# Optimization experiments

Hardware: AMD Instinct MI355X
Metric: run time of the kernel (lower is better)

The kernel has to match this reference:

```python
import jax, jax.numpy as jnp
import numpy as np

ALPHA = 0.2   # leaky relu negative slope
EPS = 1e-5    # layernorm eps
NEG = -1e12   # mask value from original code


def gat_layer(x, adj, W, a):
    # x: [N, F_in], adj: [N, N] bool, W: [F_in, F_out], a: [2*F_out, 1]
    F_out = W.shape[1]
    Wh = x @ W                                  # [N, F_out]
    # a^T [Wh_i ; Wh_j] decomposes into f1_i + f2_j (same math as the
    # O(N^2 * 2F) concat in the torch code, without materializing it)
    f1 = Wh @ a[:F_out]                         # [N, 1]
    f2 = Wh @ a[F_out:]                         # [N, 1]
    e = jax.nn.leaky_relu(f1 + f2.T, negative_slope=ALPHA)  # [N, N]
    att = jnp.where(adj, e, NEG)
    att = jax.nn.softmax(att, axis=1)           # dropout p=0.0 -> no-op
    return att @ Wh                             # [N, F_out]


def layernorm(x, g, b):
    mu = jnp.mean(x, axis=-1, keepdims=True)
    var = jnp.var(x, axis=-1, keepdims=True)
    return (x - mu) * jax.lax.rsqrt(var + EPS) * g + b


def setup_inputs() -> dict:
    N, F = 8192, 128
    key = jax.random.key(0)
    ks = jax.random.split(key, 12)
    inp = {
        "input_hs": jax.random.normal(ks[0], (2, N, F), jnp.float32),
        "adjs": jax.random.uniform(ks[1], (2, N, N)) < 0.3,   # bool adjacency
        "MPNN_emb": jax.random.normal(ks[2], (N, F), jnp.float32),
        "query": jax.random.normal(ks[3], (1, F), jnp.float32),
        # learned params (xavier-ish scale)
        "W0": jax.random.normal(ks[4], (F, F), jnp.float32) * (1.414 / np.sqrt(F)),
        "a0": jax.random.normal(ks[5], (2 * F, 1), jnp.float32) * 0.1,
        "W1": jax.random.normal(ks[6], (F, F), jnp.float32) * (1.414 / np.sqrt(F)),
        "a1": jax.random.normal(ks[7], (2 * F, 1), jnp.float32) * 0.1,
        "ln_gamma": jnp.ones((F,), jnp.float32),
        "ln_beta": jnp.zeros((F,), jnp.float32),
        "res": jax.random.normal(ks[8], (1, 1), jnp.float32) * 0.5,
    }
    return inp


def reference(input_hs, adjs, MPNN_emb, query, W0, a0, W1, a1, ln_gamma, ln_beta, res):
    h0 = gat_layer(input_hs[0], adjs[0], W0, a0)   # [N, F]
    h1 = gat_layer(input_hs[1], adjs[1], W1, a1)   # [N, F]
    q = layernorm(query, ln_gamma, ln_beta)        # [1, F]
    w1 = q @ h0.T                                  # [1, N]
    w2 = q @ h1.T
    w3 = q @ MPNN_emb.T
    scores = jax.nn.softmax(jnp.concatenate([w1, w2, w3], axis=0), axis=0)  # [3, N]
    # diag_embed(s) @ H is just per-row scaling s[:, None] * H
    mix = (scores[0][:, None] * h0
           + scores[1][:, None] * h1
           + scores[2][:, None] * MPNN_emb)
    return res * mix + input_hs[0]
```

## Files before the change

### kernel.cpp

```cpp
#include <hip/hip_runtime.h>
#include <hip/hip_bf16.h>
#include <cstdint>


#define N 8192
#define F 128
#define JS 8

typedef __attribute__((ext_vector_type(8))) short short8;
typedef __attribute__((ext_vector_type(8))) unsigned short ushort8;
typedef __attribute__((ext_vector_type(4))) float floatx4;

__device__ inline unsigned int f2bf(float x) {
  unsigned int u = __float_as_uint(x);
  u += 0x7FFFu + ((u >> 16) & 1u);
  return u >> 16;
}


__global__ __launch_bounds__(128) void k1_wh(
    const float* __restrict__ X2, const float* __restrict__ W0,
    const float* __restrict__ W1, const float* __restrict__ a0,
    const float* __restrict__ a1, unsigned short* __restrict__ Whbt,
    float* __restrict__ f1g, float* __restrict__ f2g) {
  const int l  = blockIdx.y;
  const int i0 = blockIdx.x * 16;
  const int c  = threadIdx.x;
  const float* __restrict__ X = X2 + (size_t)l * N * F + (size_t)i0 * F;
  const float* __restrict__ W = l ? W1 : W0;

  __shared__ __align__(16) float sX[16 * F];
  __shared__ float red[2][2][16];
  {
    const float4* src = (const float4*)X;
    float4* dst = (float4*)sX;
#pragma unroll
    for (int qq = 0; qq < 4; ++qq) dst[qq * 128 + c] = src[qq * 128 + c];
  }
  __syncthreads();

  float acc[16];
#pragma unroll
  for (int r = 0; r < 16; ++r) acc[r] = 0.f;

  for (int f4 = 0; f4 < 32; ++f4) {
    float w0 = W[(f4 * 4 + 0) * F + c];
    float w1 = W[(f4 * 4 + 1) * F + c];
    float w2 = W[(f4 * 4 + 2) * F + c];
    float w3 = W[(f4 * 4 + 3) * F + c];
#pragma unroll
    for (int r = 0; r < 16; ++r) {
      float4 xv = *(const float4*)(&sX[r * F + f4 * 4]);
      acc[r] = fmaf(xv.x, w0, acc[r]);
      acc[r] = fmaf(xv.y, w1, acc[r]);
      acc[r] = fmaf(xv.z, w2, acc[r]);
      acc[r] = fmaf(xv.w, w3, acc[r]);
    }
  }

  {
    unsigned short* wdst = Whbt + (size_t)l * F * N + (size_t)c * N + i0;
    ushort8 u0, u1;
#pragma unroll
    for (int r = 0; r < 8; ++r) {
      u0[r] = (unsigned short)f2bf(acc[r]);
      u1[r] = (unsigned short)f2bf(acc[8 + r]);
    }
    *(ushort8*)wdst = u0;
    *(ushort8*)(wdst + 8) = u1;
  }

  const float* __restrict__ a = l ? a1 : a0;
  const float a1c = a[c], a2c = a[F + c];
  const int w = c >> 6, lane = c & 63;
#pragma unroll
  for (int r = 0; r < 16; ++r) {
    float s1 = acc[r] * a1c;
    float s2 = acc[r] * a2c;
#pragma unroll
    for (int off = 32; off; off >>= 1) {
      s1 += __shfl_down(s1, off);
      s2 += __shfl_down(s2, off);
    }
    if (lane == 0) {
      red[w][0][r] = s1;
      red[w][1][r] = s2;
    }
  }
  __syncthreads();
  if (c < 16)
    f1g[l * N + i0 + c] = red[0][0][c] + red[1][0][c];
  else if (c < 32)
    f2g[l * N + i0 + c - 16] = red[0][1][c - 16] + red[1][1][c - 16];
}

__global__ __launch_bounds__(128) void k3_qln(
    const float* __restrict__ query, const float* __restrict__ gamma,
    const float* __restrict__ beta, float* __restrict__ qln) {
  const int t = threadIdx.x;
  float v = query[t];
  float s = v, sq = v * v;
#pragma unroll
  for (int off = 32; off; off >>= 1) {
    s += __shfl_down(s, off);
    sq += __shfl_down(sq, off);
  }
  __shared__ float sb[4];
  if ((t & 63) == 0) {
    sb[t >> 6] = s;
    sb[2 + (t >> 6)] = sq;
  }
  __syncthreads();
  float S = sb[0] + sb[1], SQ = sb[2] + sb[3];
  float mu = S * (1.f / 128.f);
  float var = SQ * (1.f / 128.f) - mu * mu;
  qln[t] = (v - mu) * rsqrtf(var + 1e-5f) * gamma[t] + beta[t];
}

__device__ inline short8 make_pfrag(float f1v, const float4& fa,
                                    const float4& fb, const int4& a0,
                                    const int4& a1, float& Lacc) {
  float p0, p1, p2, p3, p4, p5, p6, p7, sc;
  sc = f1v + fa.x; sc = fmaxf(sc, 0.2f * sc); p0 = a0.x ? __expf(sc) : 0.f;
  sc = f1v + fa.y; sc = fmaxf(sc, 0.2f * sc); p1 = a0.y ? __expf(sc) : 0.f;
  sc = f1v + fa.z; sc = fmaxf(sc, 0.2f * sc); p2 = a0.z ? __expf(sc) : 0.f;
  sc = f1v + fa.w; sc = fmaxf(sc, 0.2f * sc); p3 = a0.w ? __expf(sc) : 0.f;
  sc = f1v + fb.x; sc = fmaxf(sc, 0.2f * sc); p4 = a1.x ? __expf(sc) : 0.f;
  sc = f1v + fb.y; sc = fmaxf(sc, 0.2f * sc); p5 = a1.y ? __expf(sc) : 0.f;
  sc = f1v + fb.z; sc = fmaxf(sc, 0.2f * sc); p6 = a1.z ? __expf(sc) : 0.f;
  sc = f1v + fb.w; sc = fmaxf(sc, 0.2f * sc); p7 = a1.w ? __expf(sc) : 0.f;
  Lacc += ((p0 + p1) + (p2 + p3)) + ((p4 + p5) + (p6 + p7));
  union { unsigned int u[4]; short8 s8; } r;
  r.u[0] = f2bf(p0) | (f2bf(p1) << 16);
  r.u[1] = f2bf(p2) | (f2bf(p3) << 16);
  r.u[2] = f2bf(p4) | (f2bf(p5) << 16);
  r.u[3] = f2bf(p6) | (f2bf(p7) << 16);
  return r.s8;
}

__global__ __launch_bounds__(256) void k2_attn(
    const unsigned short* __restrict__ Whbt, const float* __restrict__ f1g,
    const float* __restrict__ f2g, const int* __restrict__ adj,
    float* __restrict__ hpart, float* __restrict__ Lpart) {
  const int l  = blockIdx.y;
  const int s  = blockIdx.z;
  const int i0 = blockIdx.x * 128;
  const int t  = threadIdx.x;
  const int wave = t >> 6, lane = t & 63;
  const int lpos = lane & 15, halfk = lane >> 4;

  const unsigned short* __restrict__ WhbL = Whbt + (size_t)l * F * N;
  const int* __restrict__ adjL = adj + (size_t)l * N * N;
  const float* __restrict__ f2L = f2g + l * N;

  const int rowA = i0 + wave * 32 + lpos;
  const float f1a = f1g[l * N + rowA];
  const float f1b = f1g[l * N + rowA + 16];
  const int* __restrict__ adjA = adjL + (size_t)rowA * N + halfk * 8;
  const int* __restrict__ adjB = adjA + (size_t)16 * N;
  const unsigned short* __restrict__ bbase = WhbL + (size_t)lpos * N + halfk * 8;
  const float* __restrict__ f2base = f2L + halfk * 8;

  floatx4 acc[2][8];
#pragma unroll
  for (int mt = 0; mt < 2; ++mt)
#pragma unroll
    for (int nt = 0; nt < 8; ++nt) acc[mt][nt] = (floatx4){0.f, 0.f, 0.f, 0.f};
  float Lacc0 = 0.f, Lacc1 = 0.f;

  const int jbeg = s * (N / JS);
  for (int jj = 0; jj < N / JS; jj += 32) {
    const int j0 = jbeg + jj;
    int4 a0 = *(const int4*)(adjA + j0);
    int4 a1 = *(const int4*)(adjA + j0 + 4);
    int4 b0 = *(const int4*)(adjB + j0);
    int4 b1 = *(const int4*)(adjB + j0 + 4);
    float4 fa = *(const float4*)(f2base + j0);
    float4 fb = *(const float4*)(f2base + j0 + 4);
    short8 bfv[8];
#pragma unroll
    for (int nt = 0; nt < 8; ++nt)
      bfv[nt] = *(const short8*)(bbase + (size_t)nt * 16 * N + j0);

    short8 af0 = make_pfrag(f1a, fa, fb, a0, a1, Lacc0);
    short8 af1 = make_pfrag(f1b, fa, fb, b0, b1, Lacc1);

#pragma unroll
    for (int nt = 0; nt < 8; ++nt) {
      acc[0][nt] = __builtin_amdgcn_mfma_f32_16x16x32_bf16(af0, bfv[nt], acc[0][nt], 0, 0, 0);
      acc[1][nt] = __builtin_amdgcn_mfma_f32_16x16x32_bf16(af1, bfv[nt], acc[1][nt], 0, 0, 0);
    }
  }

  const size_t obase = ((size_t)(l * JS + s) * N + i0) * F;
  const size_t lbase = (size_t)(l * JS + s) * N + i0;
#pragma unroll
  for (int mt = 0; mt < 2; ++mt) {
    const int rb = wave * 32 + mt * 16 + halfk * 4;
#pragma unroll
    for (int nt = 0; nt < 8; ++nt) {
#pragma unroll
      for (int reg = 0; reg < 4; ++reg)
        hpart[obase + (size_t)(rb + reg) * F + nt * 16 + lpos] = acc[mt][nt][reg];
    }
  }
  Lacc0 += __shfl_xor(Lacc0, 16);
  Lacc0 += __shfl_xor(Lacc0, 32);
  Lacc1 += __shfl_xor(Lacc1, 16);
  Lacc1 += __shfl_xor(Lacc1, 32);
  if (halfk == 0) {
    Lpart[lbase + wave * 32 + lpos] = Lacc0;
    Lpart[lbase + wave * 32 + 16 + lpos] = Lacc1;
  }
}

__global__ __launch_bounds__(256) void k4_mix(
    const float* __restrict__ hpart, const float* __restrict__ Lpart,
    const float* __restrict__ MPNN, const float* __restrict__ qln,
    const float* __restrict__ x0, const float* __restrict__ res,
    float* __restrict__ out) {
  const int row  = blockIdx.x * 4 + (threadIdx.x >> 6);
  const int lane = threadIdx.x & 63;
  const int c    = lane * 2;

  float h0x = 0.f, h0y = 0.f, h1x = 0.f, h1y = 0.f, L0 = 0.f, L1 = 0.f;
#pragma unroll
  for (int sx = 0; sx < JS; ++sx) {
    float2 v0 = *(const float2*)&hpart[((size_t)(0 * JS + sx) * N + row) * F + c];
    float2 v1 = *(const float2*)&hpart[((size_t)(1 * JS + sx) * N + row) * F + c];
    h0x += v0.x; h0y += v0.y;
    h1x += v1.x; h1y += v1.y;
    L0 += Lpart[(size_t)(0 * JS + sx) * N + row];
    L1 += Lpart[(size_t)(1 * JS + sx) * N + row];
  }
  const float i0v = 1.f / L0, i1v = 1.f / L1;
  h0x *= i0v; h0y *= i0v;
  h1x *= i1v; h1y *= i1v;

  float2 mv = *(const float2*)&MPNN[(size_t)row * F + c];
  float2 qv = *(const float2*)&qln[c];
  float w1 = qv.x * h0x + qv.y * h0y;
  float w2 = qv.x * h1x + qv.y * h1y;
  float w3 = qv.x * mv.x + qv.y * mv.y;
#pragma unroll
  for (int off = 1; off < 64; off <<= 1) {
    w1 += __shfl_xor(w1, off);
    w2 += __shfl_xor(w2, off);
    w3 += __shfl_xor(w3, off);
  }
  float m = fmaxf(w1, fmaxf(w2, w3));
  float e1 = __expf(w1 - m), e2 = __expf(w2 - m), e3 = __expf(w3 - m);
  float inv = res[0] / (e1 + e2 + e3);
  float2 xr = *(const float2*)&x0[(size_t)row * F + c];
  float2 o;
  o.x = (e1 * h0x + e2 * h1x + e3 * mv.x) * inv + xr.x;
  o.y = (e1 * h0y + e2 * h1y + e3 * mv.y) * inv + xr.y;
  *(float2*)&out[(size_t)row * F + c] = o;
}

extern "C" void kernel_launch(void* const* d_in, const int* in_sizes, int n_in,
                              void* d_out, int out_size, void* d_ws,
                              size_t ws_size, hipStream_t stream) {
  const float* x2    = (const float*)d_in[0];
  const int*   adj   = (const int*)d_in[1];
  const float* mpnn  = (const float*)d_in[2];
  const float* query = (const float*)d_in[3];
  const float* W0    = (const float*)d_in[4];
  const float* a0    = (const float*)d_in[5];
  const float* W1    = (const float*)d_in[6];
  const float* a1    = (const float*)d_in[7];
  const float* gamma = (const float*)d_in[8];
  const float* beta  = (const float*)d_in[9];
  const float* res   = (const float*)d_in[10];

  float* ws = (float*)d_ws;
  unsigned short* Whbt = (unsigned short*)ws;
  float* hpart = ws + 1048576;
  float* f1g   = ws + 17825792;
  float* f2g   = ws + 17842176;
  float* Lpart = ws + 17858560;
  float* qln   = ws + 17989632;
  float* out   = (float*)d_out;

  k1_wh<<<dim3(N / 16, 2), 128, 0, stream>>>(x2, W0, W1, a0, a1, Whbt, f1g, f2g);
  k3_qln<<<1, 128, 0, stream>>>(query, gamma, beta, qln);
  k2_attn<<<dim3(N / 128, 2, JS), 256, 0, stream>>>(Whbt, f1g, f2g, adj, hpart,
                                                    Lpart);
  k4_mix<<<N / 4, 256, 0, stream>>>(hpart, Lpart, mpnn, qln, x2, res, out);
}
```

Baseline: 836.4 us.

## Stage Wh tile in shared memory and prefetch adjacency one step ahead

The attention kernel now loads a 128x128 bf16 tile of Wh^T into padded LDS once per block, so the four waves share it instead of each fetching its B fragments from global memory. The adjacency int4 loads are software-pipelined one 32-column step ahead to hide their global latency. In exchange the kernel needs about 34KB of LDS and two barriers per tile, which may lower occupancy and add sync stalls. The kernel is likely bound by reading the int32 adjacency, so the Wh reuse may matter less than the prefetch.

```diff
diff --git a/kernel.cpp b/kernel.cpp
--- a/kernel.cpp
+++ b/kernel.cpp
@@ -149,6 +149,8 @@
   const int wave = t >> 6, lane = t & 63;
   const int lpos = lane & 15, halfk = lane >> 4;
 
+  __shared__ __align__(16) unsigned short sB[128][136];
+
   const unsigned short* __restrict__ WhbL = Whbt + (size_t)l * F * N;
   const int* __restrict__ adjL = adj + (size_t)l * N * N;
   const float* __restrict__ f2L = f2g + l * N;
@@ -158,8 +160,10 @@
   const float f1b = f1g[l * N + rowA + 16];
   const int* __restrict__ adjA = adjL + (size_t)rowA * N + halfk * 8;
   const int* __restrict__ adjB = adjA + (size_t)16 * N;
-  const unsigned short* __restrict__ bbase = WhbL + (size_t)lpos * N + halfk * 8;
   const float* __restrict__ f2base = f2L + halfk * 8;
+
+  const unsigned short* __restrict__ wsrc = WhbL + (size_t)(t >> 1) * N + (t & 1) * 8;
+  unsigned short* __restrict__ sdst = &sB[t >> 1][(t & 1) * 8];
 
   floatx4 acc[2][8];
 #pragma unroll
@@ -169,26 +173,43 @@
   float Lacc0 = 0.f, Lacc1 = 0.f;
 
   const int jbeg = s * (N / JS);
-  for (int jj = 0; jj < N / JS; jj += 32) {
-    const int j0 = jbeg + jj;
-    int4 a0 = *(const int4*)(adjA + j0);
-    int4 a1 = *(const int4*)(adjA + j0 + 4);
-    int4 b0 = *(const int4*)(adjB + j0);
-    int4 b1 = *(const int4*)(adjB + j0 + 4);
-    float4 fa = *(const float4*)(f2base + j0);
-    float4 fb = *(const float4*)(f2base + j0 + 4);
-    short8 bfv[8];
-#pragma unroll
-    for (int nt = 0; nt < 8; ++nt)
-      bfv[nt] = *(const short8*)(bbase + (size_t)nt * 16 * N + j0);
-
-    short8 af0 = make_pfrag(f1a, fa, fb, a0, a1, Lacc0);
-    short8 af1 = make_pfrag(f1b, fa, fb, b0, b1, Lacc1);
-
-#pragma unroll
-    for (int nt = 0; nt < 8; ++nt) {
-      acc[0][nt] = __builtin_amdgcn_mfma_f32_16x16x32_bf16(af0, bfv[nt], acc[0][nt], 0, 0, 0);
-      acc[1][nt] = __builtin_amdgcn_mfma_f32_16x16x32_bf16(af1, bfv[nt], acc[1][nt], 0, 0, 0);
+
+  int4 ca0 = *(const int4*)(adjA + jbeg);
+  int4 ca1 = *(const int4*)(adjA + jbeg + 4);
+  int4 cb0 = *(const int4*)(adjB + jbeg);
+  int4 cb1 = *(const int4*)(adjB + jbeg + 4);
+
+  for (int st = 0; st < (N / JS) / 128; ++st) {
+    const int jb = jbeg + st * 128;
+    __syncthreads();
+#pragma unroll
+    for (int r = 0; r < 8; ++r)
+      *(uint4*)(sdst + r * 16) = *(const uint4*)(wsrc + jb + r * 16);
+    __syncthreads();
+
+#pragma unroll
+    for (int s4 = 0; s4 < 4; ++s4) {
+      const int j0 = jb + s4 * 32;
+      int jn = j0 + 32;
+      if (jn >= jbeg + (N / JS)) jn = jbeg;
+      int4 na0 = *(const int4*)(adjA + jn);
+      int4 na1 = *(const int4*)(adjA + jn + 4);
+      int4 nb0 = *(const int4*)(adjB + jn);
+      int4 nb1 = *(const int4*)(adjB + jn + 4);
+      float4 fa = *(const float4*)(f2base + j0);
+      float4 fb = *(const float4*)(f2base + j0 + 4);
+
+      short8 af0 = make_pfrag(f1a, fa, fb, ca0, ca1, Lacc0);
+      short8 af1 = make_pfrag(f1b, fa, fb, cb0, cb1, Lacc1);
+
+      const unsigned short* bp = &sB[lpos][s4 * 32 + halfk * 8];
+#pragma unroll
+      for (int nt = 0; nt < 8; ++nt) {
+        short8 bf = *(const short8*)(bp + nt * 16 * 136);
+        acc[0][nt] = __builtin_amdgcn_mfma_f32_16x16x32_bf16(af0, bf, acc[0][nt], 0, 0, 0);
+        acc[1][nt] = __builtin_amdgcn_mfma_f32_16x16x32_bf16(af1, bf, acc[1][nt], 0, 0, 0);
+      }
+      ca0 = na0; ca1 = na1; cb0 = nb0; cb1 = nb1;
     }
   }
 
```

Result: faster. 816.5 us (-2.4%).
